# Kernel tuning notes

Hardware: AMD Instinct MI355X
Metric: run time of the kernel (lower is better)

Reference implementation:

```python
import jax, jax.numpy as jnp
import numpy as np

GRID_SIZE = 5
SPLINE_ORDER = 3
N_COEF = GRID_SIZE + SPLINE_ORDER  # 8 spline basis coefficients per input feature


def _grid(dtype):
    # grid_range = [-1, 1]; h = 2/grid_size; knots from -spline_order*h-1 to ...
    h = 2.0 / GRID_SIZE
    return (jnp.arange(-SPLINE_ORDER, GRID_SIZE + SPLINE_ORDER + 1, dtype=dtype) * h - 1.0)


def b_splines(x):
    # x: (N, in_features) -> (N, in_features, N_COEF) via Cox-de Boor recursion
    grid = _grid(x.dtype)  # (grid_size + 2*spline_order + 1,) shared across features
    xg = x[:, :, None]
    bases = ((xg >= grid[:-1]) & (xg < grid[1:])).astype(x.dtype)
    for k in range(1, SPLINE_ORDER + 1):
        left = (xg - grid[: -(k + 1)]) / (grid[k:-1] - grid[: -(k + 1)]) * bases[..., :-1]
        right = (grid[k + 1:] - xg) / (grid[k + 1:] - grid[1:-k]) * bases[..., 1:]
        bases = left + right
    return bases


def kan_linear(x, base_w, spline_w, scaler):
    # base path: silu(x) @ base_w.T ; spline path: bases contracted with scaled spline weight
    base_out = jnp.dot(jax.nn.silu(x), base_w.T)
    bases = b_splines(x)  # (N, in, C)
    sw = spline_w * scaler[:, :, None]  # (out, in, C)
    spline_out = jnp.einsum('nic,oic->no', bases, sw)
    return base_out + spline_out


def setup_inputs() -> dict:
    key = jax.random.key(0)
    ks = jax.random.split(key, 8)
    b, s, d_model, d_ff = 2, 2048, 1024, 4096
    x = jax.random.normal(ks[0], (b, s, d_model), dtype=jnp.float32)
    def mk(kw, kk, out_f, in_f):
        base_w = jax.random.normal(kw, (out_f, in_f), dtype=jnp.float32) * (1.0 / np.sqrt(in_f))
        spline_w = jax.random.normal(kk, (out_f, in_f, N_COEF), dtype=jnp.float32) * (0.1 / np.sqrt(in_f))
        scaler = jnp.ones((out_f, in_f), dtype=jnp.float32)
        return base_w, spline_w, scaler
    base_w1, spline_w1, scaler1 = mk(ks[1], ks[2], d_ff, d_model)
    base_w2, spline_w2, scaler2 = mk(ks[3], ks[4], d_model, d_ff)
    return {"x": x, "base_w1": base_w1, "spline_w1": spline_w1, "scaler1": scaler1,
            "base_w2": base_w2, "spline_w2": spline_w2, "scaler2": scaler2}


def reference(x, base_w1, spline_w1, scaler1, base_w2, spline_w2, scaler2):
    b, s, d = x.shape
    h = x.reshape(-1, d)
    h = kan_linear(h, base_w1, spline_w1, scaler1)
    h = kan_linear(h, base_w2, spline_w2, scaler2)
    return h.reshape(b, s, d)
```

## Files before the change

kernel.cpp:

```cpp
#include <hip/hip_runtime.h>


typedef unsigned short u16;
typedef __bf16 bf16x8 __attribute__((ext_vector_type(8)));
typedef float f32x4 __attribute__((ext_vector_type(4)));
typedef u16 u16x8 __attribute__((ext_vector_type(8)));

#define D_MODEL 1024
#define D_FF    4096
#define NTOK    4096
#define K1      9216
#define K2      36864
#define KCHUNK  9216

__device__ __forceinline__ u16 f2bf(float v) {
    union { float f; unsigned u; } a; a.f = v;
    unsigned r = a.u + 0x7FFFu + ((a.u >> 16) & 1u);
    return (u16)(r >> 16);
}

__device__ __forceinline__ float silu_f(float x) {
    return x / (1.f + __expf(-x));
}

__device__ __forceinline__ void llds16(const u16* g, u16* l) {
    __builtin_amdgcn_global_load_lds(
        (__attribute__((address_space(1))) void*)(u16*)g,
        (__attribute__((address_space(3))) void*)l,
        16, 0, 0);
}

__global__ __launch_bounds__(256) void build_w(
    const float* __restrict__ bw, const float* __restrict__ sw,
    const float* __restrict__ sc, u16* __restrict__ dst,
    int IN, int shift)
{
    const int idx = blockIdx.x * 256 + threadIdx.x;
    const int o = idx >> shift;
    const int i = idx & (IN - 1);
    const int rowLen = IN * 9;
    const float scv = sc[idx];
    const float* sp = sw + (size_t)idx * 8;
    f32x4 s0 = *(const f32x4*)sp;
    f32x4 s1 = *(const f32x4*)(sp + 4);
    u16x8 p;
#pragma unroll
    for (int t = 0; t < 4; ++t) {
        p[t]     = f2bf(s0[t] * scv);
        p[t + 4] = f2bf(s1[t] * scv);
    }
    dst[(size_t)o * rowLen + i] = f2bf(bw[idx]);
    *(u16x8*)(dst + (size_t)o * rowLen + IN + (size_t)i * 8) = p;
}

__global__ __launch_bounds__(128) void build_act(
    const float* __restrict__ src, int srcCols,
    u16* __restrict__ dst, int col0, int ldDst)
{
    const int g = blockIdx.x * 128 + threadIdx.x;
    const int n = blockIdx.y;
    const int base = col0 + g * 8;
    u16x8 p;
    if (base < srcCols) {
        const float* sp = src + (size_t)n * srcCols + base;
        f32x4 v0 = *(const f32x4*)sp;
        f32x4 v1 = *(const f32x4*)(sp + 4);
#pragma unroll
        for (int t = 0; t < 4; ++t) {
            p[t]     = f2bf(silu_f(v0[t]));
            p[t + 4] = f2bf(silu_f(v1[t]));
        }
    } else {
        const int i = (base - srcCols) >> 3;
        const float xv = src[(size_t)n * srcCols + i];
        const float t = (xv + 2.2f) * 2.5f;
        const bool inr = (t >= 0.f) && (t < 11.f);
        const float jf = floorf(t);
        const int j = (int)jf;
        const float f = t - jf;
        const float f2 = f * f, f3 = f2 * f;
        const float s6 = 1.f / 6.f;
        const float w3 = f3 * s6;
        const float w2 = (1.f + 3.f*f + 3.f*f2 - 3.f*f3) * s6;
        const float w1 = (4.f - 6.f*f2 + 3.f*f3) * s6;
        float w0 = 1.f - f; w0 = w0 * w0 * w0 * s6;
#pragma unroll
        for (int c = 0; c < 8; ++c) {
            float v = 0.f;
            v = (j == c)     ? w3 : v;
            v = (j == c + 1) ? w2 : v;
            v = (j == c + 2) ? w1 : v;
            v = (j == c + 3) ? w0 : v;
            v = inr ? v : 0.f;
            p[c] = f2bf(v);
        }
    }
    *(u16x8*)(dst + (size_t)n * ldDst + (size_t)g * 8) = p;
}

template <int WMODE>
__global__ __launch_bounds__(512, 2) void gemm256(
    const u16* __restrict__ A, int lda,
    const u16* __restrict__ B, int ldb,
    float* __restrict__ C, int ldc,
    int nk, size_t zstride)
{
    __shared__ __attribute__((aligned(16))) u16 sm[2][2][2][256][32];

    const int tid  = threadIdx.x;
    const int lane = tid & 63;
    const int wave = tid >> 6;
    const int wr = wave >> 2;
    const int wc = wave & 3;

    const int gx = gridDim.x, gy = gridDim.y, gz = gridDim.z;
    int flat = (blockIdx.z * gy + blockIdx.y) * gx + blockIdx.x;
    const int nwg = gx * gy * gz;
    const int cpx = nwg >> 3;
    flat = (flat & 7) * cpx + (flat >> 3);
    const int bx = flat % gx;
    const int by = (flat / gx) % gy;
    const int bz = flat / (gx * gy);

    const int m0 = by * 256;
    const int n0 = bx * 256;
    const int k0 = bz * nk * 64;

    const int sRow  = tid >> 2;
    const int swcol = ((tid & 3) ^ ((tid >> 3) & 3)) * 8;
    const u16* Ag0 = A + (size_t)(m0 + sRow)       * lda + k0 + swcol;
    const u16* Ag1 = A + (size_t)(m0 + 128 + sRow) * lda + k0 + swcol;
    const u16* Bg0 = B + (size_t)(n0 + sRow)       * ldb + k0 + swcol;
    const u16* Bg1 = B + (size_t)(n0 + 128 + sRow) * ldb + k0 + swcol;

    const int fRow = lane & 15;
    const int ucol = (((lane >> 4) ^ ((lane >> 1) & 3))) * 8;

    const f32x4 zero = {0.f, 0.f, 0.f, 0.f};
    f32x4 acc[8][4];
#pragma unroll
    for (int a = 0; a < 8; ++a)
#pragma unroll
        for (int b = 0; b < 4; ++b) acc[a][b] = zero;

#pragma unroll
    for (int p = 0; p < 4; ++p) {
        const size_t koff = (size_t)(p >> 1) * 32;
        u16* lb = &sm[0][p & 1][p >> 1][0][0] + wave * 512;
        if ((p & 1) == 0) { llds16(Ag0 + koff, lb); llds16(Ag1 + koff, lb + 4096); }
        else              { llds16(Bg0 + koff, lb); llds16(Bg1 + koff, lb + 4096); }
    }
    asm volatile("s_waitcnt vmcnt(4)" ::: "memory");
    __builtin_amdgcn_s_barrier();
    __builtin_amdgcn_sched_barrier(0);

    bf16x8 bb[4];
    for (int kt = 0; kt < nk; ++kt) {
        const int b = kt & 1;
        const int ktn = (kt + 1 < nk) ? kt + 1 : 0;
#pragma unroll
        for (int p = 0; p < 4; ++p) {
            const int ks = p >> 1, mh = p & 1;
            bf16x8 af[4];
#pragma unroll
            for (int j = 0; j < 4; ++j)
                af[j] = *(const bf16x8*)
                    &sm[b][0][ks][wr * 128 + mh * 64 + j * 16 + fRow][ucol];
            if (mh == 0) {
#pragma unroll
                for (int nf = 0; nf < 4; ++nf)
                    bb[nf] = *(const bf16x8*)
                        &sm[b][1][ks][wc * 64 + nf * 16 + fRow][ucol];
            }
            {
                const size_t koff = (size_t)ktn * 64 + (size_t)(p >> 1) * 32;
                u16* lb = &sm[b ^ 1][p & 1][p >> 1][0][0] + wave * 512;
                if ((p & 1) == 0) { llds16(Ag0 + koff, lb); llds16(Ag1 + koff, lb + 4096); }
                else              { llds16(Bg0 + koff, lb); llds16(Bg1 + koff, lb + 4096); }
            }
            asm volatile("s_waitcnt lgkmcnt(0)" ::: "memory");
            __builtin_amdgcn_sched_barrier(0);
            __builtin_amdgcn_s_setprio(1);
#pragma unroll
            for (int j = 0; j < 4; ++j)
#pragma unroll
                for (int nf = 0; nf < 4; ++nf)
                    acc[mh * 4 + j][nf] = __builtin_amdgcn_mfma_f32_16x16x32_bf16(
                        af[j], bb[nf], acc[mh * 4 + j][nf], 0, 0, 0);
            __builtin_amdgcn_s_setprio(0);
            __builtin_amdgcn_sched_barrier(0);
            if (p == 1 || p == 3)
                asm volatile("s_waitcnt vmcnt(4)" ::: "memory");
            __builtin_amdgcn_s_barrier();
            __builtin_amdgcn_sched_barrier(0);
        }
    }
    asm volatile("s_waitcnt vmcnt(0)" ::: "memory");

    float* Cz = C + (size_t)bz * zstride;
    const int cRow = m0 + wr * 128 + (lane >> 4) * 4;
    const int cCol = n0 + wc * 64 + (lane & 15);
#pragma unroll
    for (int af = 0; af < 8; ++af)
#pragma unroll
        for (int nf = 0; nf < 4; ++nf)
#pragma unroll
            for (int j = 0; j < 4; ++j) {
                const size_t off = (size_t)(cRow + af * 16 + j) * ldc
                                 + (cCol + nf * 16);
                if (WMODE == 1)      atomicAdd(&Cz[off], acc[af][nf][j]);
                else if (WMODE == 2) Cz[off] += acc[af][nf][j];
                else                 Cz[off] = acc[af][nf][j];
            }
}

__global__ __launch_bounds__(256) void reduce4(
    const float* __restrict__ z, float* __restrict__ out, int n4, int zstride4)
{
    const int i = blockIdx.x * 256 + threadIdx.x;
    if (i >= n4) return;
    const f32x4* p = (const f32x4*)z;
    f32x4 v = p[i];
    v += p[i + zstride4];
    v += p[i + 2 * zstride4];
    v += p[i + 3 * zstride4];
    *(f32x4*)(out + (size_t)i * 4) = v;
}

extern "C" void kernel_launch(void* const* d_in, const int* in_sizes, int n_in,
                              void* d_out, int out_size, void* d_ws, size_t ws_size,
                              hipStream_t stream) {
    const float* x   = (const float*)d_in[0];
    const float* bw1 = (const float*)d_in[1];
    const float* sw1 = (const float*)d_in[2];
    const float* sc1 = (const float*)d_in[3];
    const float* bw2 = (const float*)d_in[4];
    const float* sw2 = (const float*)d_in[5];
    const float* sc2 = (const float*)d_in[6];
    float* out = (float*)d_out;

    char* ws = (char*)d_ws;
    const size_t ZS = (size_t)NTOK * D_MODEL;

    if (ws_size >= 444596224ull) {
        u16*   act2  = (u16*)ws;
        u16*   act1  = (u16*)ws;
        u16*   w1    = (u16*)(ws + 75497472);
        float* hbuf  = (float*)(ws + 301989888);
        float* zbuf  = (float*)(ws + 301989888);
        u16*   w2    = (u16*)(ws + 369098752);

        build_w<<<16384, 256, 0, stream>>>(bw1, sw1, sc1, w1, D_MODEL, 10);
        build_act<<<dim3(9, NTOK), 128, 0, stream>>>(x, D_MODEL, act1, 0, K1);
        gemm256<0><<<dim3(16, 16, 1), 512, 0, stream>>>(
            act1, K1, w1, K1, hbuf, D_FF, 144, 0);

        build_w<<<16384, 256, 0, stream>>>(bw2, sw2, sc2, w2, D_FF, 12);
        build_act<<<dim3(36, NTOK), 128, 0, stream>>>(hbuf, D_FF, act2, 0, K2);
        gemm256<0><<<dim3(4, 16, 4), 512, 0, stream>>>(
            act2, K2, w2, K2, zbuf, D_MODEL, 144, ZS);
        reduce4<<<(int)(ZS / 4 / 256), 256, 0, stream>>>(
            zbuf, out, (int)(ZS / 4), (int)(ZS / 4));
        return;
    }

    u16*   regionA = (u16*)ws;
    u16*   regionB = (u16*)(ws + 75497472);
    float* hbuf    = (float*)(ws + 150994944);
    float* zbuf    = (float*)(ws + 218103808);
    const bool useZ = ws_size >= 285212672ull;

    if (!useZ)
        hipMemsetAsync(d_out, 0, ZS * sizeof(float), stream);

    build_w<<<16384, 256, 0, stream>>>(bw1, sw1, sc1, regionA, D_MODEL, 10);
    build_act<<<dim3(9, NTOK), 128, 0, stream>>>(x, D_MODEL, regionB, 0, K1);
    gemm256<0><<<dim3(16, 16, 1), 512, 0, stream>>>(
        regionB, K1, regionA, K1, hbuf, D_FF, 144, 0);

    build_w<<<16384, 256, 0, stream>>>(bw2, sw2, sc2, regionB, D_FF, 12);
    for (int ck = 0; ck < 4; ++ck) {
        build_act<<<dim3(9, NTOK), 128, 0, stream>>>(hbuf, D_FF, regionA, ck * KCHUNK, K1);
        if (useZ) {
            if (ck == 0)
                gemm256<0><<<dim3(4, 16, 4), 512, 0, stream>>>(
                    regionA, KCHUNK, regionB + (size_t)ck * KCHUNK, K2,
                    zbuf, D_MODEL, 36, ZS);
            else
                gemm256<2><<<dim3(4, 16, 4), 512, 0, stream>>>(
                    regionA, KCHUNK, regionB + (size_t)ck * KCHUNK, K2,
                    zbuf, D_MODEL, 36, ZS);
        } else {
            gemm256<1><<<dim3(4, 16, 4), 512, 0, stream>>>(
                regionA, KCHUNK, regionB + (size_t)ck * KCHUNK, K2,
                out, D_MODEL, 36, ZS);
        }
    }
    if (useZ)
        reduce4<<<(int)(ZS / 4 / 256), 256, 0, stream>>>(
            zbuf, out, (int)(ZS / 4), (int)(ZS / 4));
}
```

Baseline: 959.6 us.

## Fuse layer-2 activation build into layer-1 GEMM epilogue

Adds a GEMM epilogue mode that applies SiLU and B-spline basis expansion to layer-1 accumulators and writes the bf16 layer-2 activation matrix directly. This removes the fp32 hidden buffer round trip and the separate build_act launch when the workspace is large enough. The epilogue stores are scattered (per-element u16 and 16-byte writes at stride K2), so they may be poorly coalesced, and the extra register pressure could hurt the GEMM.

```diff
diff --git a/kernel.cpp b/kernel.cpp
--- a/kernel.cpp
+++ b/kernel.cpp
@@ -21,6 +21,32 @@
 
 __device__ __forceinline__ float silu_f(float x) {
     return x / (1.f + __expf(-x));
+}
+
+__device__ __forceinline__ u16x8 bases8(float xv) {
+    const float t = (xv + 2.2f) * 2.5f;
+    const bool inr = (t >= 0.f) && (t < 11.f);
+    const float jf = floorf(t);
+    const int j = (int)jf;
+    const float f = t - jf;
+    const float f2 = f * f, f3 = f2 * f;
+    const float s6 = 1.f / 6.f;
+    const float w3 = f3 * s6;
+    const float w2 = (1.f + 3.f*f + 3.f*f2 - 3.f*f3) * s6;
+    const float w1 = (4.f - 6.f*f2 + 3.f*f3) * s6;
+    float w0 = 1.f - f; w0 = w0 * w0 * w0 * s6;
+    u16x8 p;
+#pragma unroll
+    for (int c = 0; c < 8; ++c) {
+        float v = 0.f;
+        v = (j == c)     ? w3 : v;
+        v = (j == c + 1) ? w2 : v;
+        v = (j == c + 2) ? w1 : v;
+        v = (j == c + 3) ? w0 : v;
+        v = inr ? v : 0.f;
+        p[c] = f2bf(v);
+    }
+    return p;
 }
 
 __device__ __forceinline__ void llds16(const u16* g, u16* l) {
@@ -72,28 +98,7 @@
         }
     } else {
         const int i = (base - srcCols) >> 3;
-        const float xv = src[(size_t)n * srcCols + i];
-        const float t = (xv + 2.2f) * 2.5f;
-        const bool inr = (t >= 0.f) && (t < 11.f);
-        const float jf = floorf(t);
-        const int j = (int)jf;
-        const float f = t - jf;
-        const float f2 = f * f, f3 = f2 * f;
-        const float s6 = 1.f / 6.f;
-        const float w3 = f3 * s6;
-        const float w2 = (1.f + 3.f*f + 3.f*f2 - 3.f*f3) * s6;
-        const float w1 = (4.f - 6.f*f2 + 3.f*f3) * s6;
-        float w0 = 1.f - f; w0 = w0 * w0 * w0 * s6;
-#pragma unroll
-        for (int c = 0; c < 8; ++c) {
-            float v = 0.f;
-            v = (j == c)     ? w3 : v;
-            v = (j == c + 1) ? w2 : v;
-            v = (j == c + 2) ? w1 : v;
-            v = (j == c + 3) ? w0 : v;
-            v = inr ? v : 0.f;
-            p[c] = f2bf(v);
-        }
+        p = bases8(src[(size_t)n * srcCols + i]);
     }
     *(u16x8*)(dst + (size_t)n * ldDst + (size_t)g * 8) = p;
 }
@@ -103,7 +108,7 @@
     const u16* __restrict__ A, int lda,
     const u16* __restrict__ B, int ldb,
     float* __restrict__ C, int ldc,
-    int nk, size_t zstride)
+    int nk, size_t zstride, u16* __restrict__ actOut)
 {
     __shared__ __attribute__((aligned(16))) u16 sm[2][2][2][256][32];
 
@@ -197,21 +202,37 @@
     }
     asm volatile("s_waitcnt vmcnt(0)" ::: "memory");
 
-    float* Cz = C + (size_t)bz * zstride;
     const int cRow = m0 + wr * 128 + (lane >> 4) * 4;
     const int cCol = n0 + wc * 64 + (lane & 15);
-#pragma unroll
-    for (int af = 0; af < 8; ++af)
-#pragma unroll
-        for (int nf = 0; nf < 4; ++nf)
-#pragma unroll
-            for (int j = 0; j < 4; ++j) {
-                const size_t off = (size_t)(cRow + af * 16 + j) * ldc
-                                 + (cCol + nf * 16);
-                if (WMODE == 1)      atomicAdd(&Cz[off], acc[af][nf][j]);
-                else if (WMODE == 2) Cz[off] += acc[af][nf][j];
-                else                 Cz[off] = acc[af][nf][j];
-            }
+    if (WMODE == 3) {
+#pragma unroll
+        for (int af = 0; af < 8; ++af)
+#pragma unroll
+            for (int nf = 0; nf < 4; ++nf)
+#pragma unroll
+                for (int j = 0; j < 4; ++j) {
+                    const int row = cRow + af * 16 + j;
+                    const int col = cCol + nf * 16;
+                    const float v = acc[af][nf][j];
+                    u16* rowp = actOut + (size_t)row * K2;
+                    rowp[col] = f2bf(silu_f(v));
+                    *(u16x8*)(rowp + D_FF + (size_t)col * 8) = bases8(v);
+                }
+    } else {
+        float* Cz = C + (size_t)bz * zstride;
+#pragma unroll
+        for (int af = 0; af < 8; ++af)
+#pragma unroll
+            for (int nf = 0; nf < 4; ++nf)
+#pragma unroll
+                for (int j = 0; j < 4; ++j) {
+                    const size_t off = (size_t)(cRow + af * 16 + j) * ldc
+                                     + (cCol + nf * 16);
+                    if (WMODE == 1)      atomicAdd(&Cz[off], acc[af][nf][j]);
+                    else if (WMODE == 2) Cz[off] += acc[af][nf][j];
+                    else                 Cz[off] = acc[af][nf][j];
+                }
+    }
 }
 
 __global__ __launch_bounds__(256) void reduce4(
@@ -242,6 +263,25 @@
     char* ws = (char*)d_ws;
     const size_t ZS = (size_t)NTOK * D_MODEL;
 
+    if (ws_size >= 452984832ull) {
+        u16* act2 = (u16*)ws;
+        u16* rX   = (u16*)(ws + 301989888);
+        u16* rY   = (u16*)(ws + 377487360);
+        float* zbuf = (float*)(ws + 377487360);
+
+        build_w<<<16384, 256, 0, stream>>>(bw1, sw1, sc1, rY, D_MODEL, 10);
+        build_act<<<dim3(9, NTOK), 128, 0, stream>>>(x, D_MODEL, rX, 0, K1);
+        gemm256<3><<<dim3(16, 16, 1), 512, 0, stream>>>(
+            rX, K1, rY, K1, nullptr, 0, 144, 0, act2);
+
+        build_w<<<16384, 256, 0, stream>>>(bw2, sw2, sc2, rX, D_FF, 12);
+        gemm256<0><<<dim3(4, 16, 4), 512, 0, stream>>>(
+            act2, K2, rX, K2, zbuf, D_MODEL, 144, ZS, nullptr);
+        reduce4<<<(int)(ZS / 4 / 256), 256, 0, stream>>>(
+            zbuf, out, (int)(ZS / 4), (int)(ZS / 4));
+        return;
+    }
+
     if (ws_size >= 444596224ull) {
         u16*   act2  = (u16*)ws;
         u16*   act1  = (u16*)ws;
@@ -253,12 +293,12 @@
         build_w<<<16384, 256, 0, stream>>>(bw1, sw1, sc1, w1, D_MODEL, 10);
         build_act<<<dim3(9, NTOK), 128, 0, stream>>>(x, D_MODEL, act1, 0, K1);
         gemm256<0><<<dim3(16, 16, 1), 512, 0, stream>>>(
-            act1, K1, w1, K1, hbuf, D_FF, 144, 0);
+            act1, K1, w1, K1, hbuf, D_FF, 144, 0, nullptr);
 
         build_w<<<16384, 256, 0, stream>>>(bw2, sw2, sc2, w2, D_FF, 12);
         build_act<<<dim3(36, NTOK), 128, 0, stream>>>(hbuf, D_FF, act2, 0, K2);
         gemm256<0><<<dim3(4, 16, 4), 512, 0, stream>>>(
-            act2, K2, w2, K2, zbuf, D_MODEL, 144, ZS);
+            act2, K2, w2, K2, zbuf, D_MODEL, 144, ZS, nullptr);
         reduce4<<<(int)(ZS / 4 / 256), 256, 0, stream>>>(
             zbuf, out, (int)(ZS / 4), (int)(ZS / 4));
         return;
@@ -276,7 +316,7 @@
     build_w<<<16384, 256, 0, stream>>>(bw1, sw1, sc1, regionA, D_MODEL, 10);
     build_act<<<dim3(9, NTOK), 128, 0, stream>>>(x, D_MODEL, regionB, 0, K1);
     gemm256<0><<<dim3(16, 16, 1), 512, 0, stream>>>(
-        regionB, K1, regionA, K1, hbuf, D_FF, 144, 0);
+        regionB, K1, regionA, K1, hbuf, D_FF, 144, 0, nullptr);
 
     build_w<<<16384, 256, 0, stream>>>(bw2, sw2, sc2, regionB, D_FF, 12);
     for (int ck = 0; ck < 4; ++ck) {
@@ -285,15 +325,15 @@
             if (ck == 0)
                 gemm256<0><<<dim3(4, 16, 4), 512, 0, stream>>>(
                     regionA, KCHUNK, regionB + (size_t)ck * KCHUNK, K2,
-                    zbuf, D_MODEL, 36, ZS);
+                    zbuf, D_MODEL, 36, ZS, nullptr);
             else
                 gemm256<2><<<dim3(4, 16, 4), 512, 0, stream>>>(
                     regionA, KCHUNK, regionB + (size_t)ck * KCHUNK, K2,
-                    zbuf, D_MODEL, 36, ZS);
+                    zbuf, D_MODEL, 36, ZS, nullptr);
         } else {
             gemm256<1><<<dim3(4, 16, 4), 512, 0, stream>>>(
                 regionA, KCHUNK, regionB + (size_t)ck * KCHUNK, K2,
-                out, D_MODEL, 36, ZS);
+                out, D_MODEL, 36, ZS, nullptr);
         }
     }
     if (useZ)
```

Result: no change. 952.7 us (-0.7%).
